# Performance work log

Hardware: AMD Instinct MI355X
Metric: run time of the kernel (lower is better)

Reference implementation:

```python
import jax, jax.numpy as jnp
import numpy as np

B, L, H, V = 2048, 1024, 64, 64
LN_EPS = 1e-5
DELTA_EPS = 1e-6


def setup_inputs() -> dict:
    key = jax.random.key(0)
    ks = jax.random.split(key, 16)
    s = 0.05
    return {
        'seq': jax.random.randint(ks[0], (B, L), 0, V),
        'embed_W': jax.random.normal(ks[1], (V, H), jnp.float32),
        'ff_w1': jax.random.normal(ks[2], (H, 2 * H), jnp.float32) * s,
        'ff_b1': jnp.zeros((2 * H,), jnp.float32),
        'ff_w2': jax.random.normal(ks[3], (2 * H, H), jnp.float32) * s,
        'ff_b2': jnp.zeros((H,), jnp.float32),
        'ln_g': jnp.ones((H,), jnp.float32),
        'ln_b': jnp.zeros((H,), jnp.float32),
        'gate_w1': jax.random.normal(ks[4], (H, 16), jnp.float32) * s,
        'gate_b1': jnp.zeros((16,), jnp.float32),
        'gate_w2': jax.random.normal(ks[5], (16, 1), jnp.float32) * s,
        'gate_b2': jnp.zeros((1,), jnp.float32),
        'read_w': jax.random.normal(ks[6], (H, H), jnp.float32) * s,
        'read_b': jnp.zeros((H,), jnp.float32),
        'out_w': jax.random.normal(ks[7], (H, V), jnp.float32) * s,
        'out_b': jnp.zeros((V,), jnp.float32),
    }


def _layernorm(x, g, b):
    mu = jnp.mean(x, axis=-1, keepdims=True)
    var = jnp.var(x, axis=-1, keepdims=True)
    return (x - mu) * jax.lax.rsqrt(var + LN_EPS) * g + b


def reference(seq, embed_W, ff_w1, ff_b1, ff_w2, ff_b2, ln_g, ln_b,
              gate_w1, gate_b1, gate_w2, gate_b2, read_w, read_b, out_w, out_b):
    h = embed_W[seq]                                        # (B, L, H)
    ff = jnp.maximum(h @ ff_w1 + ff_b1, 0.0) @ ff_w2 + ff_b2
    h = _layernorm(h + ff, ln_g, ln_b)                      # (B, L, H)

    ks_seq = jnp.transpose(h[:, :-1, :], (1, 0, 2))         # (L-1, B, H) keys for scan

    def step(M, k):
        # k: (B, H); M: (B, H, H) fast-weight memory
        g = jax.nn.sigmoid(jnp.maximum(k @ gate_w1 + gate_b1, 0.0) @ gate_w2 + gate_b2)  # (B, 1)
        v_pred = jnp.einsum('bij,bj->bi', jax.lax.stop_gradient(M), k)
        denom = jnp.sum(k * k, axis=-1, keepdims=True) + DELTA_EPS
        dv = k - v_pred / denom                             # (B, H)
        dM = dv[:, :, None] * k[:, None, :]                 # outer product (B, H, H)
        return M + g[:, :, None] * dM, None

    M0 = jnp.zeros((h.shape[0], H, H), h.dtype)
    M, _ = jax.lax.scan(step, M0, ks_seq)

    q = h[:, -1, :]
    ctx = jnp.einsum('bij,bj->bi', M, q)                    # (B, H)
    logits = (ctx @ read_w + read_b) @ out_w + out_b        # (B, V)
    return logits
```

## Files before the change

### kernel.cpp

```cpp
#include <hip/hip_runtime.h>
#include <hip/hip_bf16.h>
#include <math.h>

#define Bsz 2048
#define Lsz 1024
#define Hsz 64
#define Vsz 64
#define SW  8

#define OFF_TABLE 0
#define OFF_G     4096
#define OFF_GC    8192
#define OFF_P     12288
#define OFF_WC    16384
#define OFF_GV    20480
#define OFF_C     20544
#define OFF_BC    20608

__global__ __launch_bounds__(128) void prep1_kernel(
    const float* __restrict__ embed_W, const float* __restrict__ ff_w1, const float* __restrict__ ff_b1,
    const float* __restrict__ ff_w2, const float* __restrict__ ff_b2, const float* __restrict__ ln_g,
    const float* __restrict__ ln_b, const float* __restrict__ gate_w1, const float* __restrict__ gate_b1,
    const float* __restrict__ gate_w2, const float* __restrict__ gate_b2, const float* __restrict__ read_w,
    const float* __restrict__ read_b, const float* __restrict__ out_w, const float* __restrict__ out_b,
    float* __restrict__ ws)
{
    const int tid = threadIdx.x;
    const int blk = blockIdx.x;
    if (blk < 64) {
        const int v = blk;
        __shared__ float z[128];
        __shared__ float hsh[64];
        const float* Ev = embed_W + (v << 6);
        float a = ff_b1[tid];
        #pragma unroll
        for (int i = 0; i < 64; ++i) a = fmaf(Ev[i], ff_w1[i * 128 + tid], a);
        z[tid] = fmaxf(a, 0.0f);
        __syncthreads();
        if (tid < 64) {
            float x = Ev[tid] + ff_b2[tid];
            #pragma unroll
            for (int j = 0; j < 128; ++j) x = fmaf(z[j], ff_w2[j * 64 + tid], x);
            float mu = x;
            #pragma unroll
            for (int off = 32; off > 0; off >>= 1) mu += __shfl_xor(mu, off);
            mu *= (1.0f / 64.0f);
            const float dd = x - mu;
            float var = dd * dd;
            #pragma unroll
            for (int off = 32; off > 0; off >>= 1) var += __shfl_xor(var, off);
            var *= (1.0f / 64.0f);
            const float rstd = rsqrtf(var + 1e-5f);
            const float hv = fmaf(dd * rstd, ln_g[tid], ln_b[tid]);
            ws[OFF_TABLE + (v << 6) + tid] = hv;
            hsh[tid] = hv;
            float dn = hv * hv;
            #pragma unroll
            for (int off = 32; off > 0; off >>= 1) dn += __shfl_xor(dn, off);
            dn += 1e-6f;
            float a2 = 0.0f;
            if (tid < 16) {
                float um = gate_b1[tid];
                #pragma unroll
                for (int i = 0; i < 64; ++i) um = fmaf(hsh[i], gate_w1[i * 16 + tid], um);
                a2 = fmaxf(um, 0.0f) * gate_w2[tid];
            }
            #pragma unroll
            for (int off = 8; off > 0; off >>= 1) a2 += __shfl_xor(a2, off);
            if (tid == 0) {
                a2 += gate_b2[0];
                const float g = 1.0f / (1.0f + expf(-a2));
                ws[OFF_GV + v] = g;
                ws[OFF_C + v]  = g / dn;
            }
        }
    } else if (blk < 128) {
        const int j = blk - 64;
        if (tid < 64) {
            float a = 0.0f;
            #pragma unroll
            for (int m = 0; m < 64; ++m) a = fmaf(read_w[(j << 6) + m], out_w[(m << 6) + tid], a);
            ws[OFF_WC + (j << 6) + tid] = a;
        }
    } else {
        if (tid < 64) {
            float a = out_b[tid];
            #pragma unroll
            for (int jj = 0; jj < 64; ++jj) a = fmaf(read_b[jj], out_w[(jj << 6) + tid], a);
            ws[OFF_BC + tid] = a;
        }
    }
}

__global__ __launch_bounds__(64) void prep2_kernel(float* __restrict__ ws)
{
    const int tid = threadIdx.x;
    const int blk = blockIdx.x;
    if (blk < 64) {
        const int v = blk;
        __shared__ float tT[65 * 64];
        for (int idx = tid; idx < 4096; idx += 64) {
            const int w = idx >> 6, j = idx & 63;
            tT[j * 65 + w] = ws[OFF_TABLE + idx];
        }
        __syncthreads();
        const float cv = ws[OFF_C + v];
        float a = 0.0f;
        #pragma unroll
        for (int j = 0; j < 64; ++j) a = fmaf(tT[j * 65 + v], tT[j * 65 + tid], a);
        ws[OFF_G  + (v << 6) + tid] = a;
        ws[OFF_GC + (v << 6) + tid] = cv * a;
    } else {
        const int v = blk - 64;
        float a = 0.0f;
        #pragma unroll
        for (int j = 0; j < 64; ++j)
            a = fmaf(ws[OFF_TABLE + (v << 6) + j], ws[OFF_WC + (j << 6) + tid], a);
        ws[OFF_P + (v << 6) + tid] = a;
    }
}

__global__ __launch_bounds__(SW * 64) void scan_kernel(const int* __restrict__ seq,
                                                       const float* __restrict__ ws,
                                                       float* __restrict__ out)
{
    __shared__ float ldsGc[65 * 64];
    __shared__ float ldsP[4096];
    __shared__ int   toks[SW][1024];
    __shared__ float sbuf[SW][64];
    __shared__ float ldsg[64];
    __shared__ float ldsbc[64];

    const int tid  = threadIdx.x;
    const int wave = tid >> 6;
    const int lane = tid & 63;

    for (int i = tid; i < 4096; i += SW * 64) {
        ldsGc[i] = ws[OFF_GC + i];
        ldsP[i]  = ws[OFF_P + i];
    }
    if (tid < 64) {
        ldsGc[4096 + tid] = 0.0f;
        ldsg[tid]  = ws[OFF_GV + tid];
        ldsbc[tid] = ws[OFF_BC + tid];
    }
    const int b = blockIdx.x * SW + wave;
    const int* row = seq + (size_t)b * Lsz;
    {
        int4* dst = (int4*)toks[wave];
        const int4* src = (const int4*)row;
        for (int i = lane; i < 256; i += 64) dst[i] = src[i];
    }
    __syncthreads();

    const int tokL = toks[wave][1023];
    toks[wave][1023] = 64;
    float D = ws[OFF_G + (tokL << 6) + lane];
    float u = 0.0f;

    int   tkA[16], tkB[16];
    float gcA[16], gcB[16];

    int tokvA = toks[wave][1008 + lane];
    #pragma unroll
    for (int k = 0; k < 16; ++k) {
        tkA[k] = __builtin_amdgcn_readlane(tokvA, 15 - k) & 127;
        gcA[k] = ldsGc[(tkA[k] << 6) + lane];
    }
    int tokvB = toks[wave][992 + lane];

    for (int t0 = 1023; t0 > 0; t0 -= 32) {
        #pragma unroll
        for (int k = 0; k < 16; ++k) {
            tkB[k] = __builtin_amdgcn_readlane(tokvB, 15 - k) & 127;
            gcB[k] = ldsGc[(tkB[k] << 6) + lane];
        }
        {
            const int base = t0 - 47;
            tokvA = toks[wave][(base < 0 ? 0 : base) + lane];
        }
        #pragma unroll
        for (int k = 0; k < 16; ++k) {
            const int tok = tkA[k];
            const float d = __int_as_float(
                __builtin_amdgcn_readlane(__float_as_int(D), tok));
            u += (lane == tok) ? d : 0.0f;
            D = fmaf(-d, gcA[k], D);
        }
        #pragma unroll
        for (int k = 0; k < 16; ++k) {
            tkA[k] = __builtin_amdgcn_readlane(tokvA, 15 - k) & 127;
            gcA[k] = ldsGc[(tkA[k] << 6) + lane];
        }
        {
            const int base = t0 - 63;
            tokvB = toks[wave][(base < 0 ? 0 : base) + lane];
        }
        #pragma unroll
        for (int k = 0; k < 16; ++k) {
            const int tok = tkB[k];
            const float d = __int_as_float(
                __builtin_amdgcn_readlane(__float_as_int(D), tok));
            u += (lane == tok) ? d : 0.0f;
            D = fmaf(-d, gcB[k], D);
        }
    }

    sbuf[wave][lane] = ldsg[lane] * u;
    float acc = ldsbc[lane];
    #pragma unroll 8
    for (int v = 0; v < 64; ++v)
        acc = fmaf(sbuf[wave][v], ldsP[(v << 6) + lane], acc);
    out[(size_t)b * 64 + lane] = acc;
}

extern "C" void kernel_launch(void* const* d_in, const int* in_sizes, int n_in,
                              void* d_out, int out_size, void* d_ws, size_t ws_size,
                              hipStream_t stream) {
    const int*   seq     = (const int*)  d_in[0];
    const float* embed_W = (const float*)d_in[1];
    const float* ff_w1   = (const float*)d_in[2];
    const float* ff_b1   = (const float*)d_in[3];
    const float* ff_w2   = (const float*)d_in[4];
    const float* ff_b2   = (const float*)d_in[5];
    const float* ln_g    = (const float*)d_in[6];
    const float* ln_b    = (const float*)d_in[7];
    const float* gate_w1 = (const float*)d_in[8];
    const float* gate_b1 = (const float*)d_in[9];
    const float* gate_w2 = (const float*)d_in[10];
    const float* gate_b2 = (const float*)d_in[11];
    const float* read_w  = (const float*)d_in[12];
    const float* read_b  = (const float*)d_in[13];
    const float* out_w   = (const float*)d_in[14];
    const float* out_b   = (const float*)d_in[15];
    float* ws  = (float*)d_ws;
    float* out = (float*)d_out;

    hipLaunchKernelGGL(prep1_kernel, dim3(129), dim3(128), 0, stream,
                       embed_W, ff_w1, ff_b1, ff_w2, ff_b2, ln_g, ln_b,
                       gate_w1, gate_b1, gate_w2, gate_b2, read_w, read_b,
                       out_w, out_b, ws);
    hipLaunchKernelGGL(prep2_kernel, dim3(128), dim3(64), 0, stream, ws);
    hipLaunchKernelGGL(scan_kernel, dim3(Bsz / SW), dim3(SW * 64), 0, stream,
                       seq, ws, out);
}
```

Before: 137.3 us.

## Merge prep kernels into one and tighten scan inner loop with masked add

The two preprocessing kernels become a single 64-block launch. Each block recomputes the whole embedding/FF/LayerNorm table in shared memory, then writes its own rows of G, Gc and P, which removes one launch and the global round trip between them. The scan kernel pads each token buffer with 64 sentinel entries so the clamped index arithmetic and the &127 masks go away. It also replaces the select-based accumulation of u with inline asm that uses v_cmpx to do a single masked add. The prep work is now duplicated 64 times, and the inline asm that writes exec risks interfering with compiler scheduling.

```diff
diff --git a/kernel.cpp b/kernel.cpp
--- a/kernel.cpp
+++ b/kernel.cpp
@@ -4,20 +4,15 @@
 
 #define Bsz 2048
 #define Lsz 1024
-#define Hsz 64
-#define Vsz 64
 #define SW  8
 
-#define OFF_TABLE 0
-#define OFF_G     4096
-#define OFF_GC    8192
-#define OFF_P     12288
-#define OFF_WC    16384
-#define OFF_GV    20480
-#define OFF_C     20544
-#define OFF_BC    20608
-
-__global__ __launch_bounds__(128) void prep1_kernel(
+#define OFF_G   0
+#define OFF_GC  4096
+#define OFF_P   8192
+#define OFF_GV  12288
+#define OFF_BC  12352
+
+__global__ __launch_bounds__(512) void prep_kernel(
     const float* __restrict__ embed_W, const float* __restrict__ ff_w1, const float* __restrict__ ff_b1,
     const float* __restrict__ ff_w2, const float* __restrict__ ff_b2, const float* __restrict__ ln_g,
     const float* __restrict__ ln_b, const float* __restrict__ gate_w1, const float* __restrict__ gate_b1,
@@ -25,98 +20,113 @@
     const float* __restrict__ read_b, const float* __restrict__ out_w, const float* __restrict__ out_b,
     float* __restrict__ ws)
 {
-    const int tid = threadIdx.x;
-    const int blk = blockIdx.x;
-    if (blk < 64) {
-        const int v = blk;
-        __shared__ float z[128];
-        __shared__ float hsh[64];
-        const float* Ev = embed_W + (v << 6);
-        float a = ff_b1[tid];
-        #pragma unroll
-        for (int i = 0; i < 64; ++i) a = fmaf(Ev[i], ff_w1[i * 128 + tid], a);
-        z[tid] = fmaxf(a, 0.0f);
-        __syncthreads();
-        if (tid < 64) {
-            float x = Ev[tid] + ff_b2[tid];
-            #pragma unroll
-            for (int j = 0; j < 128; ++j) x = fmaf(z[j], ff_w2[j * 64 + tid], x);
-            float mu = x;
-            #pragma unroll
-            for (int off = 32; off > 0; off >>= 1) mu += __shfl_xor(mu, off);
-            mu *= (1.0f / 64.0f);
-            const float dd = x - mu;
-            float var = dd * dd;
-            #pragma unroll
-            for (int off = 32; off > 0; off >>= 1) var += __shfl_xor(var, off);
-            var *= (1.0f / 64.0f);
-            const float rstd = rsqrtf(var + 1e-5f);
-            const float hv = fmaf(dd * rstd, ln_g[tid], ln_b[tid]);
-            ws[OFF_TABLE + (v << 6) + tid] = hv;
-            hsh[tid] = hv;
-            float dn = hv * hv;
-            #pragma unroll
-            for (int off = 32; off > 0; off >>= 1) dn += __shfl_xor(dn, off);
-            dn += 1e-6f;
-            float a2 = 0.0f;
-            if (tid < 16) {
-                float um = gate_b1[tid];
-                #pragma unroll
-                for (int i = 0; i < 64; ++i) um = fmaf(hsh[i], gate_w1[i * 16 + tid], um);
-                a2 = fmaxf(um, 0.0f) * gate_w2[tid];
-            }
-            #pragma unroll
-            for (int off = 8; off > 0; off >>= 1) a2 += __shfl_xor(a2, off);
-            if (tid == 0) {
-                a2 += gate_b2[0];
-                const float g = 1.0f / (1.0f + expf(-a2));
-                ws[OFF_GV + v] = g;
-                ws[OFF_C + v]  = g / dn;
-            }
-        }
-    } else if (blk < 128) {
-        const int j = blk - 64;
-        if (tid < 64) {
-            float a = 0.0f;
-            #pragma unroll
-            for (int m = 0; m < 64; ++m) a = fmaf(read_w[(j << 6) + m], out_w[(m << 6) + tid], a);
-            ws[OFF_WC + (j << 6) + tid] = a;
-        }
-    } else {
-        if (tid < 64) {
-            float a = out_b[tid];
-            #pragma unroll
-            for (int jj = 0; jj < 64; ++jj) a = fmaf(read_b[jj], out_w[(jj << 6) + tid], a);
-            ws[OFF_BC + tid] = a;
-        }
-    }
-}
-
-__global__ __launch_bounds__(64) void prep2_kernel(float* __restrict__ ws)
-{
-    const int tid = threadIdx.x;
-    const int blk = blockIdx.x;
-    if (blk < 64) {
-        const int v = blk;
-        __shared__ float tT[65 * 64];
-        for (int idx = tid; idx < 4096; idx += 64) {
-            const int w = idx >> 6, j = idx & 63;
-            tT[j * 65 + w] = ws[OFF_TABLE + idx];
-        }
-        __syncthreads();
-        const float cv = ws[OFF_C + v];
+    __shared__ float shE[4096];
+    __shared__ float shZ[8192];
+    __shared__ float shH[4096];
+    __shared__ float shHT[65 * 64];
+    __shared__ float shc[64];
+
+    const int tid  = threadIdx.x;
+    const int b    = blockIdx.x;
+    const int wave = tid >> 6;
+    const int lane = tid & 63;
+
+    for (int i = tid; i < 4096; i += 512) shE[i] = embed_W[i];
+    __syncthreads();
+
+    for (int idx = tid; idx < 8192; idx += 512) {
+        const int v = idx >> 7, j = idx & 127;
+        float a = ff_b1[j];
+        const float* e = &shE[v << 6];
+        #pragma unroll 8
+        for (int i = 0; i < 64; ++i) a = fmaf(e[i], ff_w1[i * 128 + j], a);
+        shZ[idx] = fmaxf(a, 0.0f);
+    }
+    __syncthreads();
+
+    for (int idx = tid; idx < 4096; idx += 512) {
+        const int v = idx >> 6, i = idx & 63;
+        float a = ff_b2[i];
+        const float* z = &shZ[v << 7];
+        #pragma unroll 8
+        for (int j = 0; j < 128; ++j) a = fmaf(z[j], ff_w2[j * 64 + i], a);
+        shH[idx] = a + shE[idx];
+    }
+    __syncthreads();
+
+    for (int v = wave; v < 64; v += 8) {
+        const float x = shH[(v << 6) + lane];
+        float mu = x;
+        #pragma unroll
+        for (int off = 32; off > 0; off >>= 1) mu += __shfl_xor(mu, off);
+        mu *= (1.0f / 64.0f);
+        const float dd = x - mu;
+        float var = dd * dd;
+        #pragma unroll
+        for (int off = 32; off > 0; off >>= 1) var += __shfl_xor(var, off);
+        var *= (1.0f / 64.0f);
+        const float rstd = rsqrtf(var + 1e-5f);
+        const float hv = fmaf(dd * rstd, ln_g[lane], ln_b[lane]);
+        shH[(v << 6) + lane] = hv;
+        shHT[lane * 65 + v]  = hv;
+        float dn = hv * hv;
+        #pragma unroll
+        for (int off = 32; off > 0; off >>= 1) dn += __shfl_xor(dn, off);
+        if (lane == 0) shc[v] = dn + 1e-6f;
+    }
+    __syncthreads();
+
+    float* shWc = shZ;
+    float* shU  = shZ + 4096;
+    for (int p = tid; p < 1024; p += 512) {
+        const int v = p >> 4, m = p & 15;
+        float um = gate_b1[m];
+        const float* hv = &shH[v << 6];
+        #pragma unroll 8
+        for (int i = 0; i < 64; ++i) um = fmaf(hv[i], gate_w1[i * 16 + m], um);
+        shU[v * 17 + m] = fmaxf(um, 0.0f) * gate_w2[m];
+    }
+    for (int idx = tid; idx < 4096; idx += 512) {
+        const int j = idx >> 6, i = idx & 63;
         float a = 0.0f;
-        #pragma unroll
-        for (int j = 0; j < 64; ++j) a = fmaf(tT[j * 65 + v], tT[j * 65 + tid], a);
-        ws[OFF_G  + (v << 6) + tid] = a;
-        ws[OFF_GC + (v << 6) + tid] = cv * a;
-    } else {
-        const int v = blk - 64;
+        #pragma unroll 8
+        for (int m = 0; m < 64; ++m) a = fmaf(read_w[(j << 6) + m], out_w[(m << 6) + i], a);
+        shWc[idx] = a;
+    }
+    __syncthreads();
+
+    if (tid < 64) {
+        const int v = tid;
+        float a2 = gate_b2[0];
+        #pragma unroll
+        for (int m = 0; m < 16; ++m) a2 += shU[v * 17 + m];
+        const float g = 1.0f / (1.0f + expf(-a2));
+        const float c = g / shc[v];
+        if (b == 0) ws[OFF_GV + v] = g;
+        shc[v] = c;
+    }
+    __syncthreads();
+
+    if (tid < 64) {
         float a = 0.0f;
-        #pragma unroll
-        for (int j = 0; j < 64; ++j)
-            a = fmaf(ws[OFF_TABLE + (v << 6) + j], ws[OFF_WC + (j << 6) + tid], a);
-        ws[OFF_P + (v << 6) + tid] = a;
+        const float* hb = &shH[b << 6];
+        #pragma unroll 8
+        for (int j = 0; j < 64; ++j) a = fmaf(hb[j], shHT[j * 65 + tid], a);
+        ws[OFF_G  + (b << 6) + tid] = a;
+        ws[OFF_GC + (b << 6) + tid] = shc[b] * a;
+    } else if (tid < 128) {
+        const int i = tid - 64;
+        float a = 0.0f;
+        const float* hb = &shH[b << 6];
+        #pragma unroll 8
+        for (int j = 0; j < 64; ++j) a = fmaf(hb[j], shWc[(j << 6) + i], a);
+        ws[OFF_P + (b << 6) + i] = a;
+    } else if (tid < 192 && b == 0) {
+        const int i = tid - 128;
+        float a = out_b[i];
+        #pragma unroll 8
+        for (int j = 0; j < 64; ++j) a = fmaf(read_b[j], out_w[(j << 6) + i], a);
+        ws[OFF_BC + i] = a;
     }
 }
 
@@ -126,7 +136,7 @@
 {
     __shared__ float ldsGc[65 * 64];
     __shared__ float ldsP[4096];
-    __shared__ int   toks[SW][1024];
+    __shared__ int   toks[SW][1104];
     __shared__ float sbuf[SW][64];
     __shared__ float ldsg[64];
     __shared__ float ldsbc[64];
@@ -135,9 +145,12 @@
     const int wave = tid >> 6;
     const int lane = tid & 63;
 
-    for (int i = tid; i < 4096; i += SW * 64) {
-        ldsGc[i] = ws[OFF_GC + i];
-        ldsP[i]  = ws[OFF_P + i];
+    {
+        const float4* srcGc = (const float4*)(ws + OFF_GC);
+        const float4* srcP  = (const float4*)(ws + OFF_P);
+        float4* dGc = (float4*)ldsGc;
+        float4* dP  = (float4*)ldsP;
+        for (int i = tid; i < 1024; i += SW * 64) { dGc[i] = srcGc[i]; dP[i] = srcP[i]; }
     }
     if (tid < 64) {
         ldsGc[4096 + tid] = 0.0f;
@@ -145,65 +158,68 @@
         ldsbc[tid] = ws[OFF_BC + tid];
     }
     const int b = blockIdx.x * SW + wave;
-    const int* row = seq + (size_t)b * Lsz;
+    int* T = toks[wave];
+    if (lane < 16) ((int4*)T)[lane] = make_int4(64, 64, 64, 64);
     {
-        int4* dst = (int4*)toks[wave];
-        const int4* src = (const int4*)row;
+        int4* dst = (int4*)(T + 64);
+        const int4* src = (const int4*)(seq + (size_t)b * Lsz);
         for (int i = lane; i < 256; i += 64) dst[i] = src[i];
     }
     __syncthreads();
 
-    const int tokL = toks[wave][1023];
-    toks[wave][1023] = 64;
+    const int tokL = T[1087];
+    T[1087] = 64;
     float D = ws[OFF_G + (tokL << 6) + lane];
     float u = 0.0f;
+    const int vlane = lane;
 
     int   tkA[16], tkB[16];
     float gcA[16], gcB[16];
 
-    int tokvA = toks[wave][1008 + lane];
+    int tokv = T[1072 + lane];
     #pragma unroll
     for (int k = 0; k < 16; ++k) {
-        tkA[k] = __builtin_amdgcn_readlane(tokvA, 15 - k) & 127;
+        tkA[k] = __builtin_amdgcn_readlane(tokv, 15 - k);
         gcA[k] = ldsGc[(tkA[k] << 6) + lane];
     }
-    int tokvB = toks[wave][992 + lane];
+    int tokvB = T[1056 + lane];
 
     for (int t0 = 1023; t0 > 0; t0 -= 32) {
         #pragma unroll
         for (int k = 0; k < 16; ++k) {
-            tkB[k] = __builtin_amdgcn_readlane(tokvB, 15 - k) & 127;
+            tkB[k] = __builtin_amdgcn_readlane(tokvB, 15 - k);
             gcB[k] = ldsGc[(tkB[k] << 6) + lane];
         }
-        {
-            const int base = t0 - 47;
-            tokvA = toks[wave][(base < 0 ? 0 : base) + lane];
-        }
-        #pragma unroll
-        for (int k = 0; k < 16; ++k) {
-            const int tok = tkA[k];
-            const float d = __int_as_float(
-                __builtin_amdgcn_readlane(__float_as_int(D), tok));
-            u += (lane == tok) ? d : 0.0f;
+        const int tokvA2 = T[t0 + 17 + lane];
+        #pragma unroll
+        for (int k = 0; k < 16; ++k) {
+            const int tok   = tkA[k];
+            const int dbits = __builtin_amdgcn_readlane(__float_as_int(D), tok);
+            const float d   = __int_as_float(dbits);
+            asm volatile("v_cmpx_eq_u32 vcc, %2, %3\n\t"
+                         "v_add_f32 %0, %1, %0\n\t"
+                         "s_mov_b64 exec, -1"
+                         : "+v"(u) : "s"(dbits), "s"(tok), "v"(vlane) : "vcc");
             D = fmaf(-d, gcA[k], D);
         }
         #pragma unroll
         for (int k = 0; k < 16; ++k) {
-            tkA[k] = __builtin_amdgcn_readlane(tokvA, 15 - k) & 127;
+            tkA[k] = __builtin_amdgcn_readlane(tokvA2, 15 - k);
             gcA[k] = ldsGc[(tkA[k] << 6) + lane];
         }
-        {
-            const int base = t0 - 63;
-            tokvB = toks[wave][(base < 0 ? 0 : base) + lane];
-        }
-        #pragma unroll
-        for (int k = 0; k < 16; ++k) {
-            const int tok = tkB[k];
-            const float d = __int_as_float(
-                __builtin_amdgcn_readlane(__float_as_int(D), tok));
-            u += (lane == tok) ? d : 0.0f;
+        const int tokvB2 = T[t0 + 1 + lane];
+        #pragma unroll
+        for (int k = 0; k < 16; ++k) {
+            const int tok   = tkB[k];
+            const int dbits = __builtin_amdgcn_readlane(__float_as_int(D), tok);
+            const float d   = __int_as_float(dbits);
+            asm volatile("v_cmpx_eq_u32 vcc, %2, %3\n\t"
+                         "v_add_f32 %0, %1, %0\n\t"
+                         "s_mov_b64 exec, -1"
+                         : "+v"(u) : "s"(dbits), "s"(tok), "v"(vlane) : "vcc");
             D = fmaf(-d, gcB[k], D);
         }
+        tokvB = tokvB2;
     }
 
     sbuf[wave][lane] = ldsg[lane] * u;
@@ -236,11 +252,10 @@
     float* ws  = (float*)d_ws;
     float* out = (float*)d_out;
 
-    hipLaunchKernelGGL(prep1_kernel, dim3(129), dim3(128), 0, stream,
+    hipLaunchKernelGGL(prep_kernel, dim3(64), dim3(512), 0, stream,
                        embed_W, ff_w1, ff_b1, ff_w2, ff_b2, ln_g, ln_b,
                        gate_w1, gate_b1, gate_w2, gate_b2, read_w, read_b,
                        out_w, out_b, ws);
-    hipLaunchKernelGGL(prep2_kernel, dim3(128), dim3(64), 0, stream, ws);
     hipLaunchKernelGGL(scan_kernel, dim3(Bsz / SW), dim3(SW * 64), 0, stream,
                        seq, ws, out);
 }
```

Result: slower. 187.3 us (+36.5%).

## Fuse prep kernels into scan kernel, recomputing tables per block

Applied to the files above, without the earlier changes.

The two precompute kernels (embedding table through FF+LayerNorm, gate values, Gram matrix, and folded readout matrix) are merged into the scan kernel. Each block now recomputes all 64-token tables redundantly in registers and LDS using cross-lane readlane broadcasts, then runs the scan. This removes two kernel launches, the workspace round trips and the serial dependency between launches. The cost is redundant prep work in every one of the 256 blocks and more LDS per block, which may reduce occupancy. The token buffer is also padded so prefetch indices no longer need clamping or masking.

```diff
diff --git a/kernel.cpp b/kernel.cpp
--- a/kernel.cpp
+++ b/kernel.cpp
@@ -4,213 +4,225 @@
 
 #define Bsz 2048
 #define Lsz 1024
-#define Hsz 64
-#define Vsz 64
 #define SW  8
 
-#define OFF_TABLE 0
-#define OFF_G     4096
-#define OFF_GC    8192
-#define OFF_P     12288
-#define OFF_WC    16384
-#define OFF_GV    20480
-#define OFF_C     20544
-#define OFF_BC    20608
-
-__global__ __launch_bounds__(128) void prep1_kernel(
+__device__ __forceinline__ float __rlf(float v, int i) {
+    return __int_as_float(__builtin_amdgcn_readlane(__float_as_int(v), i));
+}
+
+__global__ __launch_bounds__(512) void fused_kernel(
+    const int* __restrict__ seq,
     const float* __restrict__ embed_W, const float* __restrict__ ff_w1, const float* __restrict__ ff_b1,
     const float* __restrict__ ff_w2, const float* __restrict__ ff_b2, const float* __restrict__ ln_g,
     const float* __restrict__ ln_b, const float* __restrict__ gate_w1, const float* __restrict__ gate_b1,
     const float* __restrict__ gate_w2, const float* __restrict__ gate_b2, const float* __restrict__ read_w,
     const float* __restrict__ read_b, const float* __restrict__ out_w, const float* __restrict__ out_b,
-    float* __restrict__ ws)
+    float* __restrict__ out)
 {
-    const int tid = threadIdx.x;
-    const int blk = blockIdx.x;
-    if (blk < 64) {
-        const int v = blk;
-        __shared__ float z[128];
-        __shared__ float hsh[64];
-        const float* Ev = embed_W + (v << 6);
-        float a = ff_b1[tid];
-        #pragma unroll
-        for (int i = 0; i < 64; ++i) a = fmaf(Ev[i], ff_w1[i * 128 + tid], a);
-        z[tid] = fmaxf(a, 0.0f);
-        __syncthreads();
-        if (tid < 64) {
-            float x = Ev[tid] + ff_b2[tid];
-            #pragma unroll
-            for (int j = 0; j < 128; ++j) x = fmaf(z[j], ff_w2[j * 64 + tid], x);
-            float mu = x;
+    __shared__ int   toks[SW][1136];
+    __shared__ float ldsGc[65 * 64];
+    __shared__ float ldsP[64 * 64];
+    __shared__ float ldsHW[64 * 65 * 2];
+    __shared__ float ldsg[64];
+    __shared__ float ldscinv[64];
+
+    const int tid  = threadIdx.x;
+    const int wave = tid >> 6;
+    const int lane = tid & 63;
+    const int b    = blockIdx.x * SW + wave;
+
+    const int4* tsrc = (const int4*)(seq + (size_t)b * Lsz);
+    const int4 tv0 = tsrc[lane], tv1 = tsrc[64 + lane], tv2 = tsrc[128 + lane], tv3 = tsrc[192 + lane];
+
+    const int v0 = wave << 3;
+    float e[8];
+    #pragma unroll
+    for (int k = 0; k < 8; ++k) e[k] = embed_W[((v0 + k) << 6) + lane];
+
+    float za[8], zb[8];
+    {
+        const float b1a = ff_b1[lane], b1b = ff_b1[64 + lane];
+        #pragma unroll
+        for (int k = 0; k < 8; ++k) { za[k] = b1a; zb[k] = b1b; }
+    }
+    #pragma unroll 16
+    for (int i = 0; i < 64; ++i) {
+        const float w1a = ff_w1[i * 128 + lane];
+        const float w1b = ff_w1[i * 128 + 64 + lane];
+        #pragma unroll
+        for (int k = 0; k < 8; ++k) {
+            const float ei = __rlf(e[k], i);
+            za[k] = fmaf(ei, w1a, za[k]);
+            zb[k] = fmaf(ei, w1b, zb[k]);
+        }
+    }
+    #pragma unroll
+    for (int k = 0; k < 8; ++k) { za[k] = fmaxf(za[k], 0.0f); zb[k] = fmaxf(zb[k], 0.0f); }
+
+    float h[8];
+    {
+        const float b2l = ff_b2[lane];
+        #pragma unroll
+        for (int k = 0; k < 8; ++k) h[k] = e[k] + b2l;
+    }
+    #pragma unroll 16
+    for (int j = 0; j < 64; ++j) {
+        const float w2a = ff_w2[j * 64 + lane];
+        const float w2b = ff_w2[(j + 64) * 64 + lane];
+        #pragma unroll
+        for (int k = 0; k < 8; ++k) {
+            h[k] = fmaf(__rlf(za[k], j), w2a, h[k]);
+            h[k] = fmaf(__rlf(zb[k], j), w2b, h[k]);
+        }
+    }
+
+    {
+        int* T = toks[wave];
+        if (lane < 16) ((int4*)T)[lane] = make_int4(64, 64, 64, 64);
+        int4* dst = (int4*)(T + 64);
+        dst[lane] = tv0; dst[64 + lane] = tv1; dst[128 + lane] = tv2; dst[192 + lane] = tv3;
+    }
+
+    float cL[8];
+    {
+        const float lg = ln_g[lane], lb = ln_b[lane];
+        #pragma unroll
+        for (int k = 0; k < 8; ++k) {
+            float mu = h[k];
             #pragma unroll
             for (int off = 32; off > 0; off >>= 1) mu += __shfl_xor(mu, off);
             mu *= (1.0f / 64.0f);
-            const float dd = x - mu;
+            const float dd = h[k] - mu;
             float var = dd * dd;
             #pragma unroll
             for (int off = 32; off > 0; off >>= 1) var += __shfl_xor(var, off);
             var *= (1.0f / 64.0f);
             const float rstd = rsqrtf(var + 1e-5f);
-            const float hv = fmaf(dd * rstd, ln_g[tid], ln_b[tid]);
-            ws[OFF_TABLE + (v << 6) + tid] = hv;
-            hsh[tid] = hv;
+            const float hv = fmaf(dd * rstd, lg, lb);
+            h[k] = hv;
+            ldsHW[(lane * 65 + (v0 + k)) * 2] = hv;
             float dn = hv * hv;
             #pragma unroll
             for (int off = 32; off > 0; off >>= 1) dn += __shfl_xor(dn, off);
-            dn += 1e-6f;
-            float a2 = 0.0f;
-            if (tid < 16) {
-                float um = gate_b1[tid];
-                #pragma unroll
-                for (int i = 0; i < 64; ++i) um = fmaf(hsh[i], gate_w1[i * 16 + tid], um);
-                a2 = fmaxf(um, 0.0f) * gate_w2[tid];
+            cL[k] = dn + 1e-6f;
+        }
+    }
+
+    {
+        const int m = lane & 15;
+        const float gb1 = gate_b1[m], gw2v = gate_w2[m], gb2 = gate_b2[0];
+        #pragma unroll
+        for (int k = 0; k < 8; ++k) {
+            float u = gb1;
+            #pragma unroll 16
+            for (int i = 0; i < 64; ++i) u = fmaf(__rlf(h[k], i), gate_w1[i * 16 + m], u);
+            u = fmaxf(u, 0.0f) * gw2v;
+            u += __shfl_xor(u, 1); u += __shfl_xor(u, 2);
+            u += __shfl_xor(u, 4); u += __shfl_xor(u, 8);
+            const float g = 1.0f / (1.0f + __expf(-(u + gb2)));
+            if (lane == 0) { ldsg[v0 + k] = g; ldscinv[v0 + k] = cL[k] / g; }
+            cL[k] = g / cL[k];
+        }
+    }
+
+    {
+        float rw[8], wc[8];
+        #pragma unroll
+        for (int k = 0; k < 8; ++k) { rw[k] = read_w[((v0 + k) << 6) + lane]; wc[k] = 0.0f; }
+        #pragma unroll 16
+        for (int mm = 0; mm < 64; ++mm) {
+            const float ow = out_w[(mm << 6) + lane];
+            #pragma unroll
+            for (int k = 0; k < 8; ++k) wc[k] = fmaf(__rlf(rw[k], mm), ow, wc[k]);
+        }
+        #pragma unroll
+        for (int k = 0; k < 8; ++k) ldsHW[((v0 + k) * 65 + lane) * 2 + 1] = wc[k];
+    }
+    if (tid < 64) ldsGc[4096 + tid] = 0.0f;
+
+    __syncthreads();
+
+    {
+        float accG[8] = {0,0,0,0,0,0,0,0}, accP[8] = {0,0,0,0,0,0,0,0};
+        #pragma unroll 16
+        for (int j = 0; j < 64; ++j) {
+            const float2 hw = *(const float2*)&ldsHW[(j * 65 + lane) * 2];
+            #pragma unroll
+            for (int k = 0; k < 8; ++k) {
+                const float hv = __rlf(h[k], j);
+                accG[k] = fmaf(hv, hw.x, accG[k]);
+                accP[k] = fmaf(hv, hw.y, accP[k]);
             }
-            #pragma unroll
-            for (int off = 8; off > 0; off >>= 1) a2 += __shfl_xor(a2, off);
-            if (tid == 0) {
-                a2 += gate_b2[0];
-                const float g = 1.0f / (1.0f + expf(-a2));
-                ws[OFF_GV + v] = g;
-                ws[OFF_C + v]  = g / dn;
-            }
-        }
-    } else if (blk < 128) {
-        const int j = blk - 64;
-        if (tid < 64) {
-            float a = 0.0f;
-            #pragma unroll
-            for (int m = 0; m < 64; ++m) a = fmaf(read_w[(j << 6) + m], out_w[(m << 6) + tid], a);
-            ws[OFF_WC + (j << 6) + tid] = a;
-        }
-    } else {
-        if (tid < 64) {
-            float a = out_b[tid];
-            #pragma unroll
-            for (int jj = 0; jj < 64; ++jj) a = fmaf(read_b[jj], out_w[(jj << 6) + tid], a);
-            ws[OFF_BC + tid] = a;
-        }
-    }
-}
-
-__global__ __launch_bounds__(64) void prep2_kernel(float* __restrict__ ws)
-{
-    const int tid = threadIdx.x;
-    const int blk = blockIdx.x;
-    if (blk < 64) {
-        const int v = blk;
-        __shared__ float tT[65 * 64];
-        for (int idx = tid; idx < 4096; idx += 64) {
-            const int w = idx >> 6, j = idx & 63;
-            tT[j * 65 + w] = ws[OFF_TABLE + idx];
-        }
-        __syncthreads();
-        const float cv = ws[OFF_C + v];
-        float a = 0.0f;
-        #pragma unroll
-        for (int j = 0; j < 64; ++j) a = fmaf(tT[j * 65 + v], tT[j * 65 + tid], a);
-        ws[OFF_G  + (v << 6) + tid] = a;
-        ws[OFF_GC + (v << 6) + tid] = cv * a;
-    } else {
-        const int v = blk - 64;
-        float a = 0.0f;
-        #pragma unroll
-        for (int j = 0; j < 64; ++j)
-            a = fmaf(ws[OFF_TABLE + (v << 6) + j], ws[OFF_WC + (j << 6) + tid], a);
-        ws[OFF_P + (v << 6) + tid] = a;
-    }
-}
-
-__global__ __launch_bounds__(SW * 64) void scan_kernel(const int* __restrict__ seq,
-                                                       const float* __restrict__ ws,
-                                                       float* __restrict__ out)
-{
-    __shared__ float ldsGc[65 * 64];
-    __shared__ float ldsP[4096];
-    __shared__ int   toks[SW][1024];
-    __shared__ float sbuf[SW][64];
-    __shared__ float ldsg[64];
-    __shared__ float ldsbc[64];
-
-    const int tid  = threadIdx.x;
-    const int wave = tid >> 6;
-    const int lane = tid & 63;
-
-    for (int i = tid; i < 4096; i += SW * 64) {
-        ldsGc[i] = ws[OFF_GC + i];
-        ldsP[i]  = ws[OFF_P + i];
-    }
-    if (tid < 64) {
-        ldsGc[4096 + tid] = 0.0f;
-        ldsg[tid]  = ws[OFF_GV + tid];
-        ldsbc[tid] = ws[OFF_BC + tid];
-    }
-    const int b = blockIdx.x * SW + wave;
-    const int* row = seq + (size_t)b * Lsz;
-    {
-        int4* dst = (int4*)toks[wave];
-        const int4* src = (const int4*)row;
-        for (int i = lane; i < 256; i += 64) dst[i] = src[i];
-    }
+        }
+        #pragma unroll
+        for (int k = 0; k < 8; ++k) {
+            const int v = v0 + k;
+            ldsGc[(v << 6) + lane] = cL[k] * accG[k];
+            ldsP [(v << 6) + lane] = accP[k];
+        }
+    }
+
+    float bc = out_b[lane];
+    {
+        const float rb = read_b[lane];
+        #pragma unroll 16
+        for (int j = 0; j < 64; ++j) bc = fmaf(__rlf(rb, j), out_w[(j << 6) + lane], bc);
+    }
+
     __syncthreads();
 
-    const int tokL = toks[wave][1023];
-    toks[wave][1023] = 64;
-    float D = ws[OFF_G + (tokL << 6) + lane];
+    int* T = toks[wave];
+    const int tokL = T[1087];
+    T[1087] = 64;
+    float D = ldsGc[(tokL << 6) + lane] * ldscinv[tokL];
     float u = 0.0f;
 
     int   tkA[16], tkB[16];
     float gcA[16], gcB[16];
 
-    int tokvA = toks[wave][1008 + lane];
+    int tokvA = T[1072 + lane];
     #pragma unroll
     for (int k = 0; k < 16; ++k) {
-        tkA[k] = __builtin_amdgcn_readlane(tokvA, 15 - k) & 127;
+        tkA[k] = __builtin_amdgcn_readlane(tokvA, 15 - k);
         gcA[k] = ldsGc[(tkA[k] << 6) + lane];
     }
-    int tokvB = toks[wave][992 + lane];
+    int tokvB = T[1056 + lane];
 
     for (int t0 = 1023; t0 > 0; t0 -= 32) {
         #pragma unroll
         for (int k = 0; k < 16; ++k) {
-            tkB[k] = __builtin_amdgcn_readlane(tokvB, 15 - k) & 127;
+            tkB[k] = __builtin_amdgcn_readlane(tokvB, 15 - k);
             gcB[k] = ldsGc[(tkB[k] << 6) + lane];
         }
-        {
-            const int base = t0 - 47;
-            tokvA = toks[wave][(base < 0 ? 0 : base) + lane];
-        }
+        const int tokvA2 = T[t0 + 17 + lane];
         #pragma unroll
         for (int k = 0; k < 16; ++k) {
             const int tok = tkA[k];
-            const float d = __int_as_float(
-                __builtin_amdgcn_readlane(__float_as_int(D), tok));
+            const float d = __rlf(D, tok);
             u += (lane == tok) ? d : 0.0f;
             D = fmaf(-d, gcA[k], D);
         }
         #pragma unroll
         for (int k = 0; k < 16; ++k) {
-            tkA[k] = __builtin_amdgcn_readlane(tokvA, 15 - k) & 127;
+            tkA[k] = __builtin_amdgcn_readlane(tokvA2, 15 - k);
             gcA[k] = ldsGc[(tkA[k] << 6) + lane];
         }
-        {
-            const int base = t0 - 63;
-            tokvB = toks[wave][(base < 0 ? 0 : base) + lane];
-        }
+        const int tokvB2 = T[t0 + 1 + lane];
         #pragma unroll
         for (int k = 0; k < 16; ++k) {
             const int tok = tkB[k];
-            const float d = __int_as_float(
-                __builtin_amdgcn_readlane(__float_as_int(D), tok));
+            const float d = __rlf(D, tok);
             u += (lane == tok) ? d : 0.0f;
             D = fmaf(-d, gcB[k], D);
         }
-    }
-
-    sbuf[wave][lane] = ldsg[lane] * u;
-    float acc = ldsbc[lane];
-    #pragma unroll 8
+        tokvB = tokvB2;
+    }
+
+    const float s = u * ldsg[lane];
+    float acc = bc;
+    #pragma unroll 16
     for (int v = 0; v < 64; ++v)
-        acc = fmaf(sbuf[wave][v], ldsP[(v << 6) + lane], acc);
+        acc = fmaf(__rlf(s, v), ldsP[(v << 6) + lane], acc);
     out[(size_t)b * 64 + lane] = acc;
 }
 
@@ -233,14 +245,10 @@
     const float* read_b  = (const float*)d_in[13];
     const float* out_w   = (const float*)d_in[14];
     const float* out_b   = (const float*)d_in[15];
-    float* ws  = (float*)d_ws;
     float* out = (float*)d_out;
 
-    hipLaunchKernelGGL(prep1_kernel, dim3(129), dim3(128), 0, stream,
-                       embed_W, ff_w1, ff_b1, ff_w2, ff_b2, ln_g, ln_b,
+    hipLaunchKernelGGL(fused_kernel, dim3(Bsz / SW), dim3(SW * 64), 0, stream,
+                       seq, embed_W, ff_w1, ff_b1, ff_w2, ff_b2, ln_g, ln_b,
                        gate_w1, gate_b1, gate_w2, gate_b2, read_w, read_b,
-                       out_w, out_b, ws);
-    hipLaunchKernelGGL(prep2_kernel, dim3(128), dim3(64), 0, stream, ws);
-    hipLaunchKernelGGL(scan_kernel, dim3(Bsz / SW), dim3(SW * 64), 0, stream,
-                       seq, ws, out);
+                       out_w, out_b, out);
 }
```

Result: slower. 194.7 us (+41.9%).

## Pack tokens into bytes in LDS and fold gate into projection table

Applied to the files above, without the earlier changes.

The scan kernel now packs four 8-bit tokens per int in shared memory, shrinking per-wave token storage and using one LDS read per 32 tokens, with readlane and byte extraction replacing per-token reads. The gate value is folded into the output projection table in prep2. The final matvec now broadcasts u via readlane instead of a shared-memory round trip, and table loads use float4. The aim is to cut LDS footprint and instructions so occupancy and issue rate improve. The prep kernels gain odd self-assignments to workspace and every prep2 block now transposes the whole table, which adds redundant work.

```diff
diff --git a/kernel.cpp b/kernel.cpp
--- a/kernel.cpp
+++ b/kernel.cpp
@@ -4,18 +4,19 @@
 
 #define Bsz 2048
 #define Lsz 1024
-#define Hsz 64
-#define Vsz 64
 #define SW  8
 
-#define OFF_TABLE 0
-#define OFF_G     4096
-#define OFF_GC    8192
-#define OFF_P     12288
-#define OFF_WC    16384
-#define OFF_GV    20480
-#define OFF_C     20544
-#define OFF_BC    20608
+#define OFF_G   0
+#define OFF_GC  4096
+#define OFF_P   8192
+#define OFF_WC  12288
+#define OFF_GV  16384
+#define OFF_C   16448
+#define OFF_BC  16512
+
+__device__ __forceinline__ float __rlf(float v, int i) {
+    return __int_as_float(__builtin_amdgcn_readlane(__float_as_int(v), i));
+}
 
 __global__ __launch_bounds__(128) void prep1_kernel(
     const float* __restrict__ embed_W, const float* __restrict__ ff_w1, const float* __restrict__ ff_b1,
@@ -52,7 +53,8 @@
             var *= (1.0f / 64.0f);
             const float rstd = rsqrtf(var + 1e-5f);
             const float hv = fmaf(dd * rstd, ln_g[tid], ln_b[tid]);
-            ws[OFF_TABLE + (v << 6) + tid] = hv;
+            ws[OFF_G + 0] = ws[OFF_G + 0];
+            ws[ OFF_WC + 4096 + 0] = ws[OFF_WC + 4096 + 0];
             hsh[tid] = hv;
             float dn = hv * hv;
             #pragma unroll
@@ -67,6 +69,7 @@
             }
             #pragma unroll
             for (int off = 8; off > 0; off >>= 1) a2 += __shfl_xor(a2, off);
+            ws[OFF_G + (v << 6) + tid] = hv;
             if (tid == 0) {
                 a2 += gate_b2[0];
                 const float g = 1.0f / (1.0f + expf(-a2));
@@ -96,14 +99,14 @@
 {
     const int tid = threadIdx.x;
     const int blk = blockIdx.x;
+    __shared__ float tT[65 * 64];
+    for (int idx = tid; idx < 4096; idx += 64) {
+        const int w = idx >> 6, j = idx & 63;
+        tT[j * 65 + w] = ws[OFF_G + idx];
+    }
+    __syncthreads();
     if (blk < 64) {
         const int v = blk;
-        __shared__ float tT[65 * 64];
-        for (int idx = tid; idx < 4096; idx += 64) {
-            const int w = idx >> 6, j = idx & 63;
-            tT[j * 65 + w] = ws[OFF_TABLE + idx];
-        }
-        __syncthreads();
         const float cv = ws[OFF_C + v];
         float a = 0.0f;
         #pragma unroll
@@ -112,11 +115,12 @@
         ws[OFF_GC + (v << 6) + tid] = cv * a;
     } else {
         const int v = blk - 64;
+        const float gv = ws[OFF_GV + v];
         float a = 0.0f;
         #pragma unroll
         for (int j = 0; j < 64; ++j)
-            a = fmaf(ws[OFF_TABLE + (v << 6) + j], ws[OFF_WC + (j << 6) + tid], a);
-        ws[OFF_P + (v << 6) + tid] = a;
+            a = fmaf(tT[j * 65 + v], ws[OFF_WC + (j << 6) + tid], a);
+        ws[OFF_P + (v << 6) + tid] = gv * a;
     }
 }
 
@@ -125,92 +129,103 @@
                                                        float* __restrict__ out)
 {
     __shared__ float ldsGc[65 * 64];
-    __shared__ float ldsP[4096];
-    __shared__ int   toks[SW][1024];
-    __shared__ float sbuf[SW][64];
-    __shared__ float ldsg[64];
+    __shared__ float ldsPg[4096];
+    __shared__ int   pk[SW][16 + 256 + 64];
     __shared__ float ldsbc[64];
 
     const int tid  = threadIdx.x;
     const int wave = tid >> 6;
     const int lane = tid & 63;
 
-    for (int i = tid; i < 4096; i += SW * 64) {
-        ldsGc[i] = ws[OFF_GC + i];
-        ldsP[i]  = ws[OFF_P + i];
+    {
+        const float4* srcGc = (const float4*)(ws + OFF_GC);
+        const float4* srcP  = (const float4*)(ws + OFF_P);
+        float4* dGc = (float4*)ldsGc;
+        float4* dP  = (float4*)ldsPg;
+        for (int i = tid; i < 1024; i += SW * 64) { dGc[i] = srcGc[i]; dP[i] = srcP[i]; }
     }
     if (tid < 64) {
         ldsGc[4096 + tid] = 0.0f;
-        ldsg[tid]  = ws[OFF_GV + tid];
         ldsbc[tid] = ws[OFF_BC + tid];
     }
     const int b = blockIdx.x * SW + wave;
-    const int* row = seq + (size_t)b * Lsz;
+    int* P = pk[wave] + 16;
     {
-        int4* dst = (int4*)toks[wave];
-        const int4* src = (const int4*)row;
-        for (int i = lane; i < 256; i += 64) dst[i] = src[i];
+        const int4* src = (const int4*)(seq + (size_t)b * Lsz);
+        #pragma unroll
+        for (int i = 0; i < 4; ++i) {
+            const int4 tv = src[i * 64 + lane];
+            P[i * 64 + lane] = tv.x | (tv.y << 8) | (tv.z << 16) | (tv.w << 24);
+        }
+        if (lane < 16) pk[wave][lane] = 0x40404040;
     }
     __syncthreads();
 
-    const int tokL = toks[wave][1023];
-    toks[wave][1023] = 64;
+    const int lastw = P[255];
+    const int tokL  = (lastw >> 24) & 0xFF;
+    if (lane == 0) P[255] = (lastw & 0x00FFFFFF) | (64 << 24);
+
     float D = ws[OFF_G + (tokL << 6) + lane];
     float u = 0.0f;
 
     int   tkA[16], tkB[16];
     float gcA[16], gcB[16];
 
-    int tokvA = toks[wave][1008 + lane];
+    int tokv = P[248 + lane];
     #pragma unroll
-    for (int k = 0; k < 16; ++k) {
-        tkA[k] = __builtin_amdgcn_readlane(tokvA, 15 - k) & 127;
-        gcA[k] = ldsGc[(tkA[k] << 6) + lane];
-    }
-    int tokvB = toks[wave][992 + lane];
+    for (int j = 0; j < 4; ++j) {
+        const int w = __builtin_amdgcn_readlane(tokv, 7 - j);
+        tkA[4 * j + 0] = (w >> 24) & 0xFF;
+        tkA[4 * j + 1] = (w >> 16) & 0xFF;
+        tkA[4 * j + 2] = (w >>  8) & 0xFF;
+        tkA[4 * j + 3] =  w        & 0xFF;
+    }
+    #pragma unroll
+    for (int k = 0; k < 16; ++k) gcA[k] = ldsGc[(tkA[k] << 6) + lane];
 
     for (int t0 = 1023; t0 > 0; t0 -= 32) {
-        #pragma unroll
-        for (int k = 0; k < 16; ++k) {
-            tkB[k] = __builtin_amdgcn_readlane(tokvB, 15 - k) & 127;
-            gcB[k] = ldsGc[(tkB[k] << 6) + lane];
-        }
-        {
-            const int base = t0 - 47;
-            tokvA = toks[wave][(base < 0 ? 0 : base) + lane];
-        }
+        const int tokvN = P[(((t0 - 32) >> 2) - 7) + lane];
+        #pragma unroll
+        for (int j = 0; j < 4; ++j) {
+            const int w = __builtin_amdgcn_readlane(tokv, 3 - j);
+            tkB[4 * j + 0] = (w >> 24) & 0xFF;
+            tkB[4 * j + 1] = (w >> 16) & 0xFF;
+            tkB[4 * j + 2] = (w >>  8) & 0xFF;
+            tkB[4 * j + 3] =  w        & 0xFF;
+        }
+        #pragma unroll
+        for (int k = 0; k < 16; ++k) gcB[k] = ldsGc[(tkB[k] << 6) + lane];
         #pragma unroll
         for (int k = 0; k < 16; ++k) {
             const int tok = tkA[k];
-            const float d = __int_as_float(
-                __builtin_amdgcn_readlane(__float_as_int(D), tok));
+            const float d = __rlf(D, tok);
             u += (lane == tok) ? d : 0.0f;
             D = fmaf(-d, gcA[k], D);
         }
         #pragma unroll
-        for (int k = 0; k < 16; ++k) {
-            tkA[k] = __builtin_amdgcn_readlane(tokvA, 15 - k) & 127;
-            gcA[k] = ldsGc[(tkA[k] << 6) + lane];
-        }
-        {
-            const int base = t0 - 63;
-            tokvB = toks[wave][(base < 0 ? 0 : base) + lane];
-        }
+        for (int j = 0; j < 4; ++j) {
+            const int w = __builtin_amdgcn_readlane(tokvN, 7 - j);
+            tkA[4 * j + 0] = (w >> 24) & 0xFF;
+            tkA[4 * j + 1] = (w >> 16) & 0xFF;
+            tkA[4 * j + 2] = (w >>  8) & 0xFF;
+            tkA[4 * j + 3] =  w        & 0xFF;
+        }
+        #pragma unroll
+        for (int k = 0; k < 16; ++k) gcA[k] = ldsGc[(tkA[k] << 6) + lane];
         #pragma unroll
         for (int k = 0; k < 16; ++k) {
             const int tok = tkB[k];
-            const float d = __int_as_float(
-                __builtin_amdgcn_readlane(__float_as_int(D), tok));
+            const float d = __rlf(D, tok);
             u += (lane == tok) ? d : 0.0f;
             D = fmaf(-d, gcB[k], D);
         }
-    }
-
-    sbuf[wave][lane] = ldsg[lane] * u;
+        tokv = tokvN;
+    }
+
     float acc = ldsbc[lane];
-    #pragma unroll 8
+    #pragma unroll 16
     for (int v = 0; v < 64; ++v)
-        acc = fmaf(sbuf[wave][v], ldsP[(v << 6) + lane], acc);
+        acc = fmaf(__rlf(u, v), ldsPg[(v << 6) + lane], acc);
     out[(size_t)b * 64 + lane] = acc;
 }
 
```

Measured after the change: 134.6 us. About the same (-1.9%).
